# Optimization experiments

Measured on AMD Instinct MI355X. Metric: run time of the kernel, lower is better.

## Reference

```python
import jax, jax.numpy as jnp
import numpy as np

N_NODES = 40000
N_EDGES = 640000
EMB = 128
OUT_EMB = 256
NUM_DENSE = 3
NUM_TARGETS = 12
NUM_RADIAL = 6


def setup_inputs() -> dict:
    key = jax.random.key(0)
    ks = jax.random.split(key, 8)
    n_atoms = jax.random.normal(ks[0], (N_NODES, EMB), dtype=jnp.float32)
    x = jax.random.normal(ks[1], (N_EDGES, EMB), dtype=jnp.float32)
    rbf = jax.random.normal(ks[2], (N_EDGES, NUM_RADIAL), dtype=jnp.float32)
    idnb_i = jax.random.randint(ks[3], (N_EDGES,), 0, N_NODES, dtype=jnp.int64 if jax.config.read('jax_enable_x64') else jnp.int32)
    s = 0.05
    W_rbf = jax.random.normal(ks[4], (NUM_RADIAL, EMB), dtype=jnp.float32) * s
    W_up = jax.random.normal(ks[5], (EMB, OUT_EMB), dtype=jnp.float32) * s
    W_mlp = jax.random.normal(ks[6], (NUM_DENSE, OUT_EMB, OUT_EMB), dtype=jnp.float32) * s
    b_mlp = jnp.zeros((NUM_DENSE, OUT_EMB), dtype=jnp.float32)
    W_final = jax.random.normal(ks[7], (OUT_EMB, NUM_TARGETS), dtype=jnp.float32) * s
    return {"n_atoms": n_atoms, "x": x, "rbf": rbf, "idnb_i": idnb_i,
            "W_rbf": W_rbf, "W_up": W_up, "W_mlp": W_mlp, "b_mlp": b_mlp,
            "W_final": W_final}


def reference(n_atoms, x, rbf, idnb_i, W_rbf, W_up, W_mlp, b_mlp, W_final):
    # g = Dense(emb_size, no bias)(rbf): [M, EMB]
    g = rbf @ W_rbf
    # elementwise edge gate
    xe = g * x                                  # [M, EMB]
    # scatter-sum edges -> nodes (pooling_method='sum')
    pooled = jax.ops.segment_sum(xe, idnb_i, num_segments=n_atoms.shape[0])  # [N, EMB]
    # up-projection, no bias
    h = pooled @ W_up                           # [N, OUT_EMB]
    # GraphMLP: num_dense layers, swish activation, with bias
    for i in range(W_mlp.shape[0]):
        h = jax.nn.silu(h @ W_mlp[i] + b_mlp[i])
    # final output projection, no bias
    return h @ W_final                          # [N, NUM_TARGETS]
```

## Files before the change

kernel.cpp:

```cpp
#include <hip/hip_runtime.h>
#include <hip/hip_fp16.h>
#include <math.h>

constexpr int kNodes   = 40000;
constexpr int kEdges   = 640000;
constexpr int kEmb     = 128;
constexpr int kOut     = 256;
constexpr int kTargets = 12;
constexpr int kRadial  = 6;

typedef float        f32x4 __attribute__((ext_vector_type(4)));
typedef unsigned int u32x4 __attribute__((ext_vector_type(4)));

typedef __attribute__((address_space(1))) const void gvoid;
typedef __attribute__((address_space(3))) void       lvoid;

__device__ __forceinline__ unsigned short f2h(float f) {
  return __half_as_ushort(__float2half(f));
}
__device__ __forceinline__ void mfma_f16(f32x4& c, u32x4 a, u32x4 b) {
  asm volatile("v_mfma_f32_16x16x32_f16 %0, %1, %2, %0" : "+v"(c) : "v"(a), "v"(b));
}

__global__ __launch_bounds__(256) void hist_kernel(const int* __restrict__ idnb,
                                                   int* __restrict__ counts) {
  const int e = blockIdx.x * 256 + threadIdx.x;
  if (e < kEdges) atomicAdd(&counts[idnb[e]], 1);
}

__global__ __launch_bounds__(256) void scan_pass1(const int* __restrict__ counts,
                                                  int* __restrict__ bsum) {
  __shared__ int sm[256];
  const int idx = blockIdx.x * 256 + threadIdx.x;
  sm[threadIdx.x] = (idx < kNodes) ? counts[idx] : 0;
  __syncthreads();
  for (int d = 128; d > 0; d >>= 1) {
    if (threadIdx.x < d) sm[threadIdx.x] += sm[threadIdx.x + d];
    __syncthreads();
  }
  if (threadIdx.x == 0) bsum[blockIdx.x] = sm[0];
}

__global__ __launch_bounds__(256) void scan_pass3(const int* __restrict__ counts,
                                                  const int* __restrict__ bsum,
                                                  int* __restrict__ offs,
                                                  int* __restrict__ next,
                                                  int nblk) {
  __shared__ int sm[256];
  __shared__ int base;
  const int t = threadIdx.x;
  sm[t] = (t < nblk && t < (int)blockIdx.x) ? bsum[t] : 0;
  __syncthreads();
  for (int d = 128; d > 0; d >>= 1) {
    if (t < d) sm[t] += sm[t + d];
    __syncthreads();
  }
  if (t == 0) base = sm[0];
  __syncthreads();

  const int idx = blockIdx.x * 256 + t;
  const int v = (idx < kNodes) ? counts[idx] : 0;
  sm[t] = v;
  __syncthreads();
  for (int d = 1; d < 256; d <<= 1) {
    const int xsh = (t >= d) ? sm[t - d] : 0;
    __syncthreads();
    sm[t] += xsh;
    __syncthreads();
  }
  if (idx < kNodes) {
    const int e = base + sm[t] - v;
    offs[idx] = e;
    next[idx] = e;
  }
  if (blockIdx.x == 0 && t == 0) offs[kNodes] = kEdges;
}

__global__ __launch_bounds__(256) void fill_kernel(const int* __restrict__ idnb,
                                                   int* __restrict__ next,
                                                   int* __restrict__ edgeIdx) {
  const int e = blockIdx.x * 256 + threadIdx.x;
  if (e < kEdges) {
    const int p = atomicAdd(&next[idnb[e]], 1);
    edgeIdx[p] = e;
  }
}

__global__ __launch_bounds__(256) void prep_weights(
    const float* __restrict__ Wup, const float* __restrict__ Wmlp,
    const float* __restrict__ Wfin,
    unsigned short* __restrict__ WtUp, unsigned short* __restrict__ WtM,
    unsigned short* __restrict__ WtFin, int* __restrict__ counts) {
  const int id = blockIdx.x * 256 + threadIdx.x;
  if (id < kNodes) counts[id] = 0;

  if (id < 32768) {
    const int e = id & 7, u = id >> 3;
    const int l = u & 63, j = (u >> 6) & 3, wv = (u >> 8) & 3, c = u >> 10;
    const int n = wv * 64 + j * 16 + (l & 15);
    const int k = c * 32 + (l >> 4) * 8 + e;
    WtUp[id] = f2h(Wup[k * 256 + n]);
    return;
  }
  const int id2 = id - 32768;
  if (id2 < 3 * 65536) {
    const int L = id2 >> 16, r = id2 & 65535;
    const int e = r & 7, u = r >> 3;
    const int l = u & 63, j = (u >> 6) & 3, wv = (u >> 8) & 3, c = u >> 10;
    const int n = wv * 64 + j * 16 + (l & 15);
    const int k = c * 32 + (l >> 4) * 8 + e;
    WtM[id2] = f2h(Wmlp[L * 65536 + k * 256 + n]);
    return;
  }
  const int id3 = id2 - 3 * 65536;
  if (id3 < 16 * 256) {
    const int n = id3 >> 8, k = id3 & 255;
    WtFin[id3] = (n < kTargets) ? f2h(Wfin[k * kTargets + n]) : (unsigned short)0;
  }
}

__global__ __launch_bounds__(256) void gather_kernel(
    const float* __restrict__ x, const float* __restrict__ rbf,
    const int* __restrict__ offs, const int* __restrict__ edgeIdx,
    const float* __restrict__ W_rbf, unsigned short* __restrict__ pooled) {
  __shared__ float wLds[kRadial * kEmb];
  for (int i = threadIdx.x; i < kRadial * kEmb; i += 256) wLds[i] = W_rbf[i];
  __syncthreads();

  const int sub = threadIdx.x & 31;
  const int n   = blockIdx.x * 8 + (threadIdx.x >> 5);

  f32x4 w[kRadial];
#pragma unroll
  for (int j = 0; j < kRadial; ++j)
    w[j] = *(const f32x4*)(wLds + j * kEmb + sub * 4);

  const int beg = offs[n], end = offs[n + 1];
  f32x4 acc = {0.f, 0.f, 0.f, 0.f};

  for (int i = beg; i < end; ++i) {
    const int e = edgeIdx[i];
    const float* rr = rbf + (size_t)e * kRadial;
    const float r0 = rr[0], r1 = rr[1], r2 = rr[2];
    const float r3 = rr[3], r4 = rr[4], r5 = rr[5];
    const f32x4 xv =
        __builtin_nontemporal_load((const f32x4*)(x + (size_t)e * kEmb + sub * 4));
    const f32x4 g = r0 * w[0] + r1 * w[1] + r2 * w[2] +
                    r3 * w[3] + r4 * w[4] + r5 * w[5];
    acc += g * xv;
  }
  ushort4 hv;
  hv.x = f2h(acc.x);
  hv.y = f2h(acc.y);
  hv.z = f2h(acc.z);
  hv.w = f2h(acc.w);
  *(ushort4*)(pooled + (size_t)n * kEmb + sub * 4) = hv;
}

__global__ __launch_bounds__(256) void fused_mlp(
    const unsigned short* __restrict__ pooled,
    const unsigned short* __restrict__ WtUp,
    const unsigned short* __restrict__ WtM,
    const unsigned short* __restrict__ WtFin,
    const float* __restrict__ b_mlp, float* __restrict__ out) {
  __shared__ unsigned short act[64][266];
  __shared__ unsigned short sB[2][8192];

  const int tid     = threadIdx.x;
  const int rowBase = blockIdx.x * 64;
  const int w    = tid >> 6;
  const int lane = tid & 63;
  const int lrow = lane & 15;
  const int kgrp = lane >> 4;

#pragma unroll
  for (int p = 0; p < 4; ++p) {
    const int q = p * 256 + tid;
    const int r = q >> 4, c = q & 15;
    *(u32x4*)&act[r][c * 8] =
        *(const u32x4*)(pooled + (size_t)(rowBase + r) * kEmb + c * 8);
  }
  __syncthreads();

  for (int l = 0; l < 4; ++l) {
    const int nc = (l == 0) ? 4 : 8;
    const unsigned short* W = (l == 0) ? WtUp : WtM + (size_t)(l - 1) * 65536;

    float bj[4] = {0.f, 0.f, 0.f, 0.f};
    if (l >= 1) {
      const float* bias = b_mlp + (size_t)(l - 1) * kOut;
#pragma unroll
      for (int j = 0; j < 4; ++j) bj[j] = bias[w * 64 + j * 16 + lrow];
      asm volatile("" ::"v"(bj[0]), "v"(bj[1]), "v"(bj[2]), "v"(bj[3]));
    }

#pragma unroll
    for (int j = 0; j < 4; ++j)
      __builtin_amdgcn_global_load_lds(
          (gvoid*)(W + w * 2048 + j * 512 + lane * 8),
          (lvoid*)&sB[0][w * 2048 + j * 512], 16, 0, 0);

    f32x4 acc[4][4];
#pragma unroll
    for (int i = 0; i < 4; ++i)
#pragma unroll
      for (int j = 0; j < 4; ++j) acc[i][j] = f32x4{0.f, 0.f, 0.f, 0.f};

    int buf = 0;
    for (int c = 0; c < nc; ++c) {
      if (c + 1 < nc) {
        const unsigned short* Wn = W + (size_t)(c + 1) * 8192;
#pragma unroll
        for (int j = 0; j < 4; ++j)
          __builtin_amdgcn_global_load_lds(
              (gvoid*)(Wn + w * 2048 + j * 512 + lane * 8),
              (lvoid*)&sB[buf ^ 1][w * 2048 + j * 512], 16, 0, 0);
        asm volatile("s_waitcnt vmcnt(4)" ::: "memory");
      } else {
        asm volatile("s_waitcnt vmcnt(0)" ::: "memory");
      }
      u32x4 a[4], b[4];
#pragma unroll
      for (int i = 0; i < 4; ++i)
        a[i] = *(const u32x4*)&act[i * 16 + lrow][c * 32 + kgrp * 8];
#pragma unroll
      for (int j = 0; j < 4; ++j)
        b[j] = *(const u32x4*)&sB[buf][w * 2048 + j * 512 + lane * 8];
      __builtin_amdgcn_s_setprio(1);
#pragma unroll
      for (int j = 0; j < 4; ++j)
#pragma unroll
        for (int i = 0; i < 4; ++i) mfma_f16(acc[i][j], a[i], b[j]);
      __builtin_amdgcn_s_setprio(0);
      buf ^= 1;
    }

    __syncthreads();
#pragma unroll
    for (int j = 0; j < 4; ++j) {
      const int col = w * 64 + j * 16 + lrow;
#pragma unroll
      for (int i = 0; i < 4; ++i) {
#pragma unroll
        for (int r = 0; r < 4; ++r) {
          float v = acc[i][j][r];
          if (l >= 1) {
            v += bj[j];
            v = v / (1.f + __expf(-v));
          }
          act[i * 16 + kgrp * 4 + r][col] = f2h(v);
        }
      }
    }
    __syncthreads();
  }

  unsigned short (*sWf)[266] = (unsigned short(*)[266]) & sB[0][0];
  float (*sPart)[64][16]     = (float(*)[64][16]) & sB[1][0];
#pragma unroll
  for (int p = 0; p < 2; ++p) {
    const int q = p * 256 + tid;
    const int n = q >> 5, c = q & 31;
    *(u32x4*)&sWf[n][c * 8] = *(const u32x4*)(WtFin + (size_t)n * 256 + c * 8);
  }
  __syncthreads();

  f32x4 accF[4];
#pragma unroll
  for (int i = 0; i < 4; ++i) accF[i] = f32x4{0.f, 0.f, 0.f, 0.f};
#pragma unroll
  for (int s = 0; s < 2; ++s) {
    const int cc = w * 2 + s;
    const u32x4 b = *(const u32x4*)&sWf[lrow][cc * 32 + kgrp * 8];
#pragma unroll
    for (int i = 0; i < 4; ++i) {
      const u32x4 a = *(const u32x4*)&act[i * 16 + lrow][cc * 32 + kgrp * 8];
      mfma_f16(accF[i], a, b);
    }
  }
#pragma unroll
  for (int i = 0; i < 4; ++i)
#pragma unroll
    for (int r = 0; r < 4; ++r)
      sPart[w][i * 16 + kgrp * 4 + r][lrow] = accF[i][r];
  __syncthreads();

  for (int q = tid; q < 64 * kTargets; q += 256) {
    const int r = q / kTargets, t = q % kTargets;
    out[(size_t)(rowBase + r) * kTargets + t] =
        sPart[0][r][t] + sPart[1][r][t] + sPart[2][r][t] + sPart[3][r][t];
  }
}

extern "C" void kernel_launch(void* const* d_in, const int* in_sizes, int n_in,
                              void* d_out, int out_size, void* d_ws, size_t ws_size,
                              hipStream_t stream) {
  const float* x      = (const float*)d_in[1];
  const float* rbf    = (const float*)d_in[2];
  const int*   idnb   = (const int*)d_in[3];
  const float* W_rbf  = (const float*)d_in[4];
  const float* W_up   = (const float*)d_in[5];
  const float* W_mlp  = (const float*)d_in[6];
  const float* b_mlp  = (const float*)d_in[7];
  const float* W_fin  = (const float*)d_in[8];
  float* out = (float*)d_out;

  char* wp = (char*)d_ws;
  auto alloc = [&](size_t bytes) -> void* {
    void* r = wp;
    wp += (bytes + 255) & ~(size_t)255;
    return r;
  };
  unsigned short* pooled = (unsigned short*)alloc((size_t)kNodes * kEmb * 2);
  unsigned short* WtUp   = (unsigned short*)alloc(32768 * 2);
  unsigned short* WtM    = (unsigned short*)alloc(3 * 65536 * 2);
  unsigned short* WtFin  = (unsigned short*)alloc(16 * 256 * 2);
  int* counts  = (int*)alloc((size_t)kNodes * 4);
  int* offs    = (int*)alloc((size_t)(kNodes + 8) * 4);
  int* next    = (int*)alloc((size_t)kNodes * 4);
  int* edgeIdx = (int*)alloc((size_t)kEdges * 4);
  int* bsum    = (int*)alloc(256 * 4);

  constexpr int nScanBlk = (kNodes + 255) / 256;
  constexpr int prepElems = 32768 + 3 * 65536 + 16 * 256;

  prep_weights<<<(prepElems + 255) / 256, 256, 0, stream>>>(
      W_up, W_mlp, W_fin, WtUp, WtM, WtFin, counts);

  hist_kernel<<<kEdges / 256, 256, 0, stream>>>(idnb, counts);
  scan_pass1<<<nScanBlk, 256, 0, stream>>>(counts, bsum);
  scan_pass3<<<nScanBlk, 256, 0, stream>>>(counts, bsum, offs, next, nScanBlk);
  fill_kernel<<<kEdges / 256, 256, 0, stream>>>(idnb, next, edgeIdx);

  gather_kernel<<<kNodes / 8, 256, 0, stream>>>(x, rbf, offs, edgeIdx, W_rbf,
                                                pooled);

  fused_mlp<<<kNodes / 64, 256, 0, stream>>>(pooled, WtUp, WtM, WtFin, b_mlp,
                                             out);
}
```

Before: 221.2 us.

## Fuse edge gather into MLP kernel and use single-block scan

Measured after the change: 449.5 us. 2.03x slower.

```diff
diff --git a/kernel.cpp b/kernel.cpp
--- a/kernel.cpp
+++ b/kernel.cpp
@@ -20,70 +20,6 @@
 }
 __device__ __forceinline__ void mfma_f16(f32x4& c, u32x4 a, u32x4 b) {
   asm volatile("v_mfma_f32_16x16x32_f16 %0, %1, %2, %0" : "+v"(c) : "v"(a), "v"(b));
-}
-
-__global__ __launch_bounds__(256) void hist_kernel(const int* __restrict__ idnb,
-                                                   int* __restrict__ counts) {
-  const int e = blockIdx.x * 256 + threadIdx.x;
-  if (e < kEdges) atomicAdd(&counts[idnb[e]], 1);
-}
-
-__global__ __launch_bounds__(256) void scan_pass1(const int* __restrict__ counts,
-                                                  int* __restrict__ bsum) {
-  __shared__ int sm[256];
-  const int idx = blockIdx.x * 256 + threadIdx.x;
-  sm[threadIdx.x] = (idx < kNodes) ? counts[idx] : 0;
-  __syncthreads();
-  for (int d = 128; d > 0; d >>= 1) {
-    if (threadIdx.x < d) sm[threadIdx.x] += sm[threadIdx.x + d];
-    __syncthreads();
-  }
-  if (threadIdx.x == 0) bsum[blockIdx.x] = sm[0];
-}
-
-__global__ __launch_bounds__(256) void scan_pass3(const int* __restrict__ counts,
-                                                  const int* __restrict__ bsum,
-                                                  int* __restrict__ offs,
-                                                  int* __restrict__ next,
-                                                  int nblk) {
-  __shared__ int sm[256];
-  __shared__ int base;
-  const int t = threadIdx.x;
-  sm[t] = (t < nblk && t < (int)blockIdx.x) ? bsum[t] : 0;
-  __syncthreads();
-  for (int d = 128; d > 0; d >>= 1) {
-    if (t < d) sm[t] += sm[t + d];
-    __syncthreads();
-  }
-  if (t == 0) base = sm[0];
-  __syncthreads();
-
-  const int idx = blockIdx.x * 256 + t;
-  const int v = (idx < kNodes) ? counts[idx] : 0;
-  sm[t] = v;
-  __syncthreads();
-  for (int d = 1; d < 256; d <<= 1) {
-    const int xsh = (t >= d) ? sm[t - d] : 0;
-    __syncthreads();
-    sm[t] += xsh;
-    __syncthreads();
-  }
-  if (idx < kNodes) {
-    const int e = base + sm[t] - v;
-    offs[idx] = e;
-    next[idx] = e;
-  }
-  if (blockIdx.x == 0 && t == 0) offs[kNodes] = kEdges;
-}
-
-__global__ __launch_bounds__(256) void fill_kernel(const int* __restrict__ idnb,
-                                                   int* __restrict__ next,
-                                                   int* __restrict__ edgeIdx) {
-  const int e = blockIdx.x * 256 + threadIdx.x;
-  if (e < kEdges) {
-    const int p = atomicAdd(&next[idnb[e]], 1);
-    edgeIdx[p] = e;
-  }
 }
 
 __global__ __launch_bounds__(256) void prep_weights(
@@ -119,52 +55,70 @@
   }
 }
 
-__global__ __launch_bounds__(256) void gather_kernel(
+__global__ __launch_bounds__(256) void hist_kernel(const int* __restrict__ idnb,
+                                                   int* __restrict__ counts) {
+  const int e = blockIdx.x * 256 + threadIdx.x;
+  if (e < kEdges) atomicAdd(&counts[idnb[e]], 1);
+}
+
+__global__ __launch_bounds__(1024) void scan_block(const int* __restrict__ counts,
+                                                   int* __restrict__ offs,
+                                                   int* __restrict__ next) {
+  __shared__ int sm[1024];
+  const int t = threadIdx.x;
+  constexpr int C = 40;
+  const int base = t * C;
+  int loc[C];
+  int s = 0;
+#pragma unroll
+  for (int i = 0; i < C; ++i) {
+    const int idx = base + i;
+    const int v = (idx < kNodes) ? counts[idx] : 0;
+    loc[i] = s;
+    s += v;
+  }
+  sm[t] = s;
+  __syncthreads();
+  for (int d = 1; d < 1024; d <<= 1) {
+    const int v = (t >= d) ? sm[t - d] : 0;
+    __syncthreads();
+    sm[t] += v;
+    __syncthreads();
+  }
+  const int excl = (t == 0) ? 0 : sm[t - 1];
+#pragma unroll
+  for (int i = 0; i < C; ++i) {
+    const int idx = base + i;
+    if (idx < kNodes) {
+      const int e = excl + loc[i];
+      offs[idx] = e;
+      next[idx] = e;
+    }
+  }
+  if (t == 0) offs[kNodes] = kEdges;
+}
+
+__global__ __launch_bounds__(256) void fill_kernel(const int* __restrict__ idnb,
+                                                   int* __restrict__ next,
+                                                   int* __restrict__ edgeIdx) {
+  const int e = blockIdx.x * 256 + threadIdx.x;
+  if (e < kEdges) {
+    const int p = atomicAdd(&next[idnb[e]], 1);
+    edgeIdx[p] = e;
+  }
+}
+
+__global__ __launch_bounds__(256) void gather_mlp(
     const float* __restrict__ x, const float* __restrict__ rbf,
     const int* __restrict__ offs, const int* __restrict__ edgeIdx,
-    const float* __restrict__ W_rbf, unsigned short* __restrict__ pooled) {
-  __shared__ float wLds[kRadial * kEmb];
-  for (int i = threadIdx.x; i < kRadial * kEmb; i += 256) wLds[i] = W_rbf[i];
-  __syncthreads();
-
-  const int sub = threadIdx.x & 31;
-  const int n   = blockIdx.x * 8 + (threadIdx.x >> 5);
-
-  f32x4 w[kRadial];
-#pragma unroll
-  for (int j = 0; j < kRadial; ++j)
-    w[j] = *(const f32x4*)(wLds + j * kEmb + sub * 4);
-
-  const int beg = offs[n], end = offs[n + 1];
-  f32x4 acc = {0.f, 0.f, 0.f, 0.f};
-
-  for (int i = beg; i < end; ++i) {
-    const int e = edgeIdx[i];
-    const float* rr = rbf + (size_t)e * kRadial;
-    const float r0 = rr[0], r1 = rr[1], r2 = rr[2];
-    const float r3 = rr[3], r4 = rr[4], r5 = rr[5];
-    const f32x4 xv =
-        __builtin_nontemporal_load((const f32x4*)(x + (size_t)e * kEmb + sub * 4));
-    const f32x4 g = r0 * w[0] + r1 * w[1] + r2 * w[2] +
-                    r3 * w[3] + r4 * w[4] + r5 * w[5];
-    acc += g * xv;
-  }
-  ushort4 hv;
-  hv.x = f2h(acc.x);
-  hv.y = f2h(acc.y);
-  hv.z = f2h(acc.z);
-  hv.w = f2h(acc.w);
-  *(ushort4*)(pooled + (size_t)n * kEmb + sub * 4) = hv;
-}
-
-__global__ __launch_bounds__(256) void fused_mlp(
-    const unsigned short* __restrict__ pooled,
+    const float* __restrict__ W_rbf,
     const unsigned short* __restrict__ WtUp,
     const unsigned short* __restrict__ WtM,
     const unsigned short* __restrict__ WtFin,
     const float* __restrict__ b_mlp, float* __restrict__ out) {
   __shared__ unsigned short act[64][266];
   __shared__ unsigned short sB[2][8192];
+  __shared__ float wLds[kRadial * kEmb];
 
   const int tid     = threadIdx.x;
   const int rowBase = blockIdx.x * 64;
@@ -174,11 +128,43 @@
   const int kgrp = lane >> 4;
 
 #pragma unroll
-  for (int p = 0; p < 4; ++p) {
-    const int q = p * 256 + tid;
-    const int r = q >> 4, c = q & 15;
-    *(u32x4*)&act[r][c * 8] =
-        *(const u32x4*)(pooled + (size_t)(rowBase + r) * kEmb + c * 8);
+  for (int j = 0; j < 4; ++j)
+    __builtin_amdgcn_global_load_lds(
+        (gvoid*)(WtUp + w * 2048 + j * 512 + lane * 8),
+        (lvoid*)&sB[0][w * 2048 + j * 512], 16, 0, 0);
+
+  for (int i = tid; i < kRadial * kEmb; i += 256) wLds[i] = W_rbf[i];
+  __syncthreads();
+
+  {
+    const int sub = tid & 31;
+    const int grp = tid >> 5;
+    f32x4 wreg[kRadial];
+#pragma unroll
+    for (int j = 0; j < kRadial; ++j)
+      wreg[j] = *(const f32x4*)(wLds + j * kEmb + sub * 4);
+
+    for (int q = 0; q < 8; ++q) {
+      const int n = rowBase + grp * 8 + q;
+      const int beg = offs[n], end = offs[n + 1];
+      f32x4 acc = {0.f, 0.f, 0.f, 0.f};
+      for (int i = beg; i < end; ++i) {
+        const int e = edgeIdx[i];
+        const float* rr = rbf + (size_t)e * kRadial;
+        const float r0 = rr[0], r1 = rr[1], r2 = rr[2];
+        const float r3 = rr[3], r4 = rr[4], r5 = rr[5];
+        const f32x4 xv = __builtin_nontemporal_load(
+            (const f32x4*)(x + (size_t)e * kEmb + sub * 4));
+        const f32x4 g = r0 * wreg[0] + r1 * wreg[1] + r2 * wreg[2] +
+                        r3 * wreg[3] + r4 * wreg[4] + r5 * wreg[5];
+        acc += g * xv;
+      }
+      ushort2 h0, h1;
+      h0.x = f2h(acc.x); h0.y = f2h(acc.y);
+      h1.x = f2h(acc.z); h1.y = f2h(acc.w);
+      *(ushort2*)&act[grp * 8 + q][sub * 4]     = h0;
+      *(ushort2*)&act[grp * 8 + q][sub * 4 + 2] = h1;
+    }
   }
   __syncthreads();
 
@@ -194,11 +180,13 @@
       asm volatile("" ::"v"(bj[0]), "v"(bj[1]), "v"(bj[2]), "v"(bj[3]));
     }
 
-#pragma unroll
-    for (int j = 0; j < 4; ++j)
-      __builtin_amdgcn_global_load_lds(
-          (gvoid*)(W + w * 2048 + j * 512 + lane * 8),
-          (lvoid*)&sB[0][w * 2048 + j * 512], 16, 0, 0);
+    if (l >= 1) {
+#pragma unroll
+      for (int j = 0; j < 4; ++j)
+        __builtin_amdgcn_global_load_lds(
+            (gvoid*)(W + w * 2048 + j * 512 + lane * 8),
+            (lvoid*)&sB[0][w * 2048 + j * 512], 16, 0, 0);
+    }
 
     f32x4 acc[4][4];
 #pragma unroll
@@ -311,7 +299,6 @@
     wp += (bytes + 255) & ~(size_t)255;
     return r;
   };
-  unsigned short* pooled = (unsigned short*)alloc((size_t)kNodes * kEmb * 2);
   unsigned short* WtUp   = (unsigned short*)alloc(32768 * 2);
   unsigned short* WtM    = (unsigned short*)alloc(3 * 65536 * 2);
   unsigned short* WtFin  = (unsigned short*)alloc(16 * 256 * 2);
@@ -319,22 +306,14 @@
   int* offs    = (int*)alloc((size_t)(kNodes + 8) * 4);
   int* next    = (int*)alloc((size_t)kNodes * 4);
   int* edgeIdx = (int*)alloc((size_t)kEdges * 4);
-  int* bsum    = (int*)alloc(256 * 4);
-
-  constexpr int nScanBlk = (kNodes + 255) / 256;
+
   constexpr int prepElems = 32768 + 3 * 65536 + 16 * 256;
 
   prep_weights<<<(prepElems + 255) / 256, 256, 0, stream>>>(
       W_up, W_mlp, W_fin, WtUp, WtM, WtFin, counts);
-
   hist_kernel<<<kEdges / 256, 256, 0, stream>>>(idnb, counts);
-  scan_pass1<<<nScanBlk, 256, 0, stream>>>(counts, bsum);
-  scan_pass3<<<nScanBlk, 256, 0, stream>>>(counts, bsum, offs, next, nScanBlk);
+  scan_block<<<1, 1024, 0, stream>>>(counts, offs, next);
   fill_kernel<<<kEdges / 256, 256, 0, stream>>>(idnb, next, edgeIdx);
-
-  gather_kernel<<<kNodes / 8, 256, 0, stream>>>(x, rbf, offs, edgeIdx, W_rbf,
-                                                pooled);
-
-  fused_mlp<<<kNodes / 64, 256, 0, stream>>>(pooled, WtUp, WtM, WtFin, b_mlp,
-                                             out);
-}
+  gather_mlp<<<kNodes / 64, 256, 0, stream>>>(x, rbf, offs, edgeIdx, W_rbf,
+                                              WtUp, WtM, WtFin, b_mlp, out);
+}
```
